# Kernel tuning notes

Measured on AMD Instinct MI355X. Metric: run time of the kernel, lower is better.

## Reference

```python
import jax, jax.numpy as jnp
import numpy as np

EPS = 1e-5
KP_EXTENT = 0.05


def _lrelu(x):
    return jnp.where(x >= 0, x, 0.1 * x)


def _bn(x, g, b, m, v):
    return g * (x - m) * jax.lax.rsqrt(v + EPS) + b


def setup_inputs() -> dict:
    key = jax.random.key(0)
    ks = jax.random.split(key, 20)
    N, K, P = 40000, 32, 15
    C_in, mid, C_out = 128, 64, 256
    inp = {}
    inp["features"] = jax.random.normal(ks[0], (N, C_in), dtype=jnp.float32)
    # points in a small cube so neighbor distances ~ KP_radius (0.06)
    inp["points"] = jax.random.uniform(ks[1], (N, 3), dtype=jnp.float32) * 0.1
    inp["neighbor_idx"] = jax.random.randint(ks[2], (N, K), 0, N, dtype=jnp.int32)
    # main path: Conv1D(in->mid) + BN
    inp["W1"] = jax.random.normal(ks[3], (C_in, mid), dtype=jnp.float32) * (1.0 / np.sqrt(C_in))
    inp["bn1_g"] = 1.0 + 0.1 * jax.random.normal(ks[4], (mid,), dtype=jnp.float32)
    inp["bn1_b"] = 0.1 * jax.random.normal(ks[5], (mid,), dtype=jnp.float32)
    inp["bn1_m"] = 0.1 * jax.random.normal(ks[6], (mid,), dtype=jnp.float32)
    inp["bn1_v"] = 0.5 + 0.5 * jax.random.uniform(ks[7], (mid,), dtype=jnp.float32)
    # KPConv: fixed kernel point positions in ball of radius 0.06, weights [P, mid, mid]
    inp["kernel_points"] = jax.random.normal(ks[8], (P, 3), dtype=jnp.float32) * 0.03
    inp["Wkp"] = jax.random.normal(ks[9], (P, mid, mid), dtype=jnp.float32) * (1.0 / np.sqrt(P * mid))
    # Conv1D(mid->out) + BN
    inp["W2"] = jax.random.normal(ks[10], (mid, C_out), dtype=jnp.float32) * (1.0 / np.sqrt(mid))
    inp["bn2_g"] = 1.0 + 0.1 * jax.random.normal(ks[11], (C_out,), dtype=jnp.float32)
    inp["bn2_b"] = 0.1 * jax.random.normal(ks[12], (C_out,), dtype=jnp.float32)
    inp["bn2_m"] = 0.1 * jax.random.normal(ks[13], (C_out,), dtype=jnp.float32)
    inp["bn2_v"] = 0.5 + 0.5 * jax.random.uniform(ks[14], (C_out,), dtype=jnp.float32)
    # shortcut Conv1D(in->out) + BN
    inp["Ws"] = jax.random.normal(ks[15], (C_in, C_out), dtype=jnp.float32) * (1.0 / np.sqrt(C_in))
    inp["bns_g"] = 1.0 + 0.1 * jax.random.normal(ks[16], (C_out,), dtype=jnp.float32)
    inp["bns_b"] = 0.1 * jax.random.normal(ks[17], (C_out,), dtype=jnp.float32)
    inp["bns_m"] = 0.1 * jax.random.normal(ks[18], (C_out,), dtype=jnp.float32)
    inp["bns_v"] = 0.5 + 0.5 * jax.random.uniform(ks[19], (C_out,), dtype=jnp.float32)
    return inp


def reference(features, points, neighbor_idx,
              W1, bn1_g, bn1_b, bn1_m, bn1_v,
              kernel_points, Wkp,
              W2, bn2_g, bn2_b, bn2_m, bn2_v,
              Ws, bns_g, bns_b, bns_m, bns_v):
    # --- main path ---
    # Conv1D: pointwise linear + BN(eval) + LeakyReLU
    x = _lrelu(_bn(features @ W1, bn1_g, bn1_b, bn1_m, bn1_v))  # [N, mid]
    # KPConvNeighbors (rigid KPConv, linear influence)
    f_n = x[neighbor_idx]                                # [N, K, mid] gather
    d = points[neighbor_idx] - points[:, None, :]        # [N, K, 3]
    diff = d[:, :, None, :] - kernel_points[None, None]  # [N, K, P, 3]
    dist = jnp.sqrt(jnp.sum(diff * diff, axis=-1))       # [N, K, P]
    h = jnp.maximum(0.0, 1.0 - dist / KP_EXTENT)         # influence [N, K, P]
    wf = jnp.einsum('nkp,nkc->npc', h, f_n)              # [N, P, mid]
    y = jnp.einsum('npc,pcd->nd', wf, Wkp)               # [N, mid]
    y = _lrelu(y)
    y = _lrelu(_bn(y @ W2, bn2_g, bn2_b, bn2_m, bn2_v))  # [N, C_out]
    # --- shortcut ---
    sc = _lrelu(_bn(features @ Ws, bns_g, bns_b, bns_m, bns_v))
    # residual add + final leaky relu
    return _lrelu(y + sc)
```

## Files before the change

### kernel.cpp

```cpp
#include <hip/hip_runtime.h>
#include <math.h>

#define EPSBN 1e-5f

constexpr int CIN  = 128;
constexpr int MID  = 64;
constexpr int COUT = 256;
constexpr int KNB  = 32;
constexpr int PKP  = 15;

constexpr int PSTR = 72;
constexpr int WROW = PKP * PSTR;
constexpr int YROW = 72;

typedef __bf16 v8bf  __attribute__((ext_vector_type(8)));
typedef float  f32x4 __attribute__((ext_vector_type(4)));

__device__ __forceinline__ float lrelu(float x) { return x >= 0.0f ? x : 0.1f * x; }

__device__ __forceinline__ void split1(float v, unsigned short& h, unsigned short& l) {
    __bf16 hb = (__bf16)v;
    float r = v - (float)hb;
    __bf16 lb = (__bf16)r;
    h = __builtin_bit_cast(unsigned short, hb);
    l = __builtin_bit_cast(unsigned short, lb);
}

__device__ __forceinline__ void split_frag8(const float* s, v8bf& hi, v8bf& lo) {
    #pragma unroll
    for (int j = 0; j < 8; ++j) {
        __bf16 hb = (__bf16)s[j];
        float r = s[j] - (float)hb;
        hi[j] = hb;
        lo[j] = (__bf16)r;
    }
}

__device__ __forceinline__ v8bf as_v8bf(uint4 u) {
    union { uint4 u; v8bf v; } X;
    X.u = u;
    return X.v;
}

__device__ __forceinline__ unsigned bf16_rne(float f) {
    unsigned u = __float_as_uint(f);
    return (u + 0x7fffu + ((u >> 16) & 1u)) >> 16;
}
__device__ __forceinline__ void split_pack8(const float* s, v8bf& hi, v8bf& lo) {
    unsigned h[8], l[8];
    #pragma unroll
    for (int j = 0; j < 8; ++j) {
        float a = s[j];
        unsigned hu = bf16_rne(a);
        float r = a - __uint_as_float(hu << 16);
        h[j] = hu;
        l[j] = bf16_rne(r);
    }
    union { uint4 u; v8bf v; } H, L;
    H.u = make_uint4(h[0] | (h[1] << 16), h[2] | (h[3] << 16),
                     h[4] | (h[5] << 16), h[6] | (h[7] << 16));
    L.u = make_uint4(l[0] | (l[1] << 16), l[2] | (l[3] << 16),
                     l[4] | (l[5] << 16), l[6] | (l[7] << 16));
    hi = H.v;
    lo = L.v;
}

__global__ __launch_bounds__(256) void prep(
    const float* __restrict__ Wkp, const float* __restrict__ W1,
    const float* __restrict__ Ws,  const float* __restrict__ W2,
    const float* __restrict__ g1, const float* __restrict__ b1,
    const float* __restrict__ m1, const float* __restrict__ v1,
    const float* __restrict__ gs, const float* __restrict__ bs,
    const float* __restrict__ ms, const float* __restrict__ vs,
    const float* __restrict__ g2, const float* __restrict__ b2,
    const float* __restrict__ m2, const float* __restrict__ v2,
    uint4* __restrict__ WkpPh, uint4* __restrict__ WkpPl,
    uint4* __restrict__ WcPh,  uint4* __restrict__ WcPl,
    uint4* __restrict__ W2Ph,  uint4* __restrict__ W2Pl,
    float* __restrict__ bnscale, float* __restrict__ bnshift)
{
    const int b = blockIdx.x, t = threadIdx.x;
    if (b < 30) {
        int gt = b * 256 + t;
        int lane = gt & 63, rest = gt >> 6;
        int nt = rest & 3, kt = rest >> 2;
        int col = nt * 16 + (lane & 15);
        int kbase = kt * 32 + ((lane >> 4) << 3);
        float tmp[8];
        #pragma unroll
        for (int j = 0; j < 8; ++j)
            tmp[j] = Wkp[(size_t)(kbase + j) * MID + col];
        v8bf hi, lo;
        split_pack8(tmp, hi, lo);
        union { v8bf v; uint4 u; } H, L; H.v = hi; L.v = lo;
        WkpPh[gt] = H.u; WkpPl[gt] = L.u;
    } else if (b < 50) {
        int gt = (b - 30) * 256 + t;
        int lane = gt & 63, rest = gt >> 6;
        int kt = rest / 20, nt = rest % 20;
        int c = nt * 16 + (lane & 15);
        int kbase = kt * 32 + ((lane >> 4) << 3);
        float tmp[8];
        #pragma unroll
        for (int j = 0; j < 8; ++j) {
            int k = kbase + j;
            tmp[j] = (c < 64) ? W1[(size_t)k * MID + c]
                              : Ws[(size_t)k * COUT + (c - 64)];
        }
        v8bf hi, lo;
        split_pack8(tmp, hi, lo);
        union { v8bf v; uint4 u; } H, L; H.v = hi; L.v = lo;
        WcPh[gt] = H.u; WcPl[gt] = L.u;
    } else if (b < 58) {
        int gt = (b - 50) * 256 + t;
        int lane = gt & 63, rest = gt >> 6;
        int kt = rest >> 4, nt = rest & 15;
        int col = nt * 16 + (lane & 15);
        int kbase = kt * 32 + ((lane >> 4) << 3);
        float tmp[8];
        #pragma unroll
        for (int j = 0; j < 8; ++j)
            tmp[j] = W2[(size_t)(kbase + j) * COUT + col];
        v8bf hi, lo;
        split_pack8(tmp, hi, lo);
        union { v8bf v; uint4 u; } H, L; H.v = hi; L.v = lo;
        W2Ph[gt] = H.u; W2Pl[gt] = L.u;
    } else {
        int v = (b - 58) * 256 + t;
        if (v < 576) {
            float g, bb, mm, vv;
            if (v < 64)       { g = g1[v]; bb = b1[v]; mm = m1[v]; vv = v1[v]; }
            else if (v < 320) { int c = v - 64;  g = gs[c]; bb = bs[c]; mm = ms[c]; vv = vs[c]; }
            else              { int c = v - 320; g = g2[c]; bb = b2[c]; mm = m2[c]; vv = v2[c]; }
            float s = g / sqrtf(vv + EPSBN);
            bnscale[v] = s;
            bnshift[v] = bb - mm * s;
        }
    }
}

__global__ __launch_bounds__(256) void k1_mfma(
    const float* __restrict__ F,
    const uint4* __restrict__ WcPh, const uint4* __restrict__ WcPl,
    const float* __restrict__ bnscale, const float* __restrict__ bnshift,
    unsigned* __restrict__ xp, float* __restrict__ scbuf)
{
    __shared__ float As[64][132];
    const int t = threadIdx.x;
    const int n0 = blockIdx.x * 64;

    const float4* src = (const float4*)(F + (size_t)n0 * CIN);
    #pragma unroll
    for (int i = 0; i < 8; ++i) {
        int idx = t + 256 * i;
        int row = idx >> 5, c4 = idx & 31;
        float4 v = src[idx];
        *(float4*)&As[row][c4 * 4] = v;
    }
    __syncthreads();

    const int l = t & 63, w = t >> 6;
    const int arow = w * 16 + (l & 15);
    const int k8 = (l >> 4) * 8;

    f32x4 acc[20];
    #pragma unroll
    for (int nt = 0; nt < 20; ++nt) acc[nt] = (f32x4){0.f, 0.f, 0.f, 0.f};

    #pragma unroll
    for (int kt = 0; kt < 4; ++kt) {
        float tmp[8];
        const float* ap = &As[arow][kt * 32 + k8];
        #pragma unroll
        for (int j = 0; j < 8; ++j) tmp[j] = ap[j];
        v8bf ah, al;
        split_frag8(tmp, ah, al);
        #pragma unroll
        for (int nt = 0; nt < 20; ++nt) {
            int bidx = ((kt * 20 + nt) << 6) + l;
            v8bf bh = as_v8bf(WcPh[bidx]);
            v8bf bl = as_v8bf(WcPl[bidx]);
            acc[nt] = __builtin_amdgcn_mfma_f32_16x16x32_bf16(ah, bh, acc[nt], 0, 0, 0);
            acc[nt] = __builtin_amdgcn_mfma_f32_16x16x32_bf16(al, bh, acc[nt], 0, 0, 0);
            acc[nt] = __builtin_amdgcn_mfma_f32_16x16x32_bf16(ah, bl, acc[nt], 0, 0, 0);
        }
    }

    const int colr = l & 15;
    const int rq = (l >> 4) * 4;
    #pragma unroll
    for (int nt = 0; nt < 20; ++nt) {
        int col = nt * 16 + colr;
        float sc = bnscale[col], sh = bnshift[col];
        #pragma unroll
        for (int r = 0; r < 4; ++r) {
            int row = n0 + w * 16 + rq + r;
            float val = lrelu(acc[nt][r] * sc + sh);
            if (col < 64) {
                unsigned short hu, lu;
                split1(val, hu, lu);
                xp[(size_t)row * MID + col] = ((unsigned)hu << 16) | lu;
            } else {
                scbuf[(size_t)row * COUT + (col - 64)] = val;
            }
        }
    }
}

__global__ __launch_bounds__(256) void k234_fused(
    const unsigned* __restrict__ xp,
    const float* __restrict__ pts,
    const int* __restrict__ nidx,
    const float* __restrict__ kpp,
    const uint4* __restrict__ WkpPh, const uint4* __restrict__ WkpPl,
    const uint4* __restrict__ W2Ph,  const uint4* __restrict__ W2Pl,
    const float* __restrict__ bnscale, const float* __restrict__ bnshift,
    const float* __restrict__ scbuf,
    float* __restrict__ out)
{
    __shared__ unsigned short wfsH[16 * WROW];
    __shared__ unsigned short wfsL[16 * WROW];
    __shared__ unsigned short yH[16 * YROW];
    __shared__ unsigned short yL[16 * YROW];

    const int t = threadIdx.x;
    const int l = t & 63, w = t >> 6;
    const int col = l & 15, kg = l >> 4;
    const int k8 = kg * 8;
    const int n0 = blockIdx.x * 16;

    float kx = 0.f, ky = 0.f, kz = 0.f;
    if (col < PKP) { kx = kpp[col * 3]; ky = kpp[col * 3 + 1]; kz = kpp[col * 3 + 2]; }

    for (int pt = 0; pt < 4; ++pt) {
        const int pl = w * 4 + pt;
        const int n  = n0 + pl;
        const float cx = pts[(size_t)n * 3];
        const float cy = pts[(size_t)n * 3 + 1];
        const float cz = pts[(size_t)n * 3 + 2];
        const int4 nba = ((const int4*)nidx)[(size_t)n * 8 + kg * 2];
        const int4 nbb = ((const int4*)nidx)[(size_t)n * 8 + kg * 2 + 1];
        int nb[8] = {nba.x, nba.y, nba.z, nba.w, nbb.x, nbb.y, nbb.z, nbb.w};

        unsigned u[8][4];
        #pragma unroll
        for (int j = 0; j < 8; ++j) {
            const unsigned* xr = xp + (size_t)nb[j] * MID + col;
            u[j][0] = xr[0];
            u[j][1] = xr[16];
            u[j][2] = xr[32];
            u[j][3] = xr[48];
        }

        float hv[8];
        #pragma unroll
        for (int j = 0; j < 8; ++j) {
            float ex = (pts[(size_t)nb[j] * 3]     - cx) - kx;
            float ey = (pts[(size_t)nb[j] * 3 + 1] - cy) - ky;
            float ez = (pts[(size_t)nb[j] * 3 + 2] - cz) - kz;
            float dist = sqrtf(ex * ex + ey * ey + ez * ez);
            float h = fmaxf(0.0f, 1.0f - dist * 20.0f);
            hv[j] = (col < PKP) ? h : 0.0f;
        }
        v8bf ah, al;
        split_frag8(hv, ah, al);

        #pragma unroll
        for (int nt = 0; nt < 4; ++nt) {
            unsigned bhW[4], blW[4];
            #pragma unroll
            for (int i = 0; i < 4; ++i) {
                unsigned u0 = u[2 * i][nt], u1 = u[2 * i + 1][nt];
                bhW[i] = (u1 & 0xFFFF0000u) | (u0 >> 16);
                blW[i] = (u1 << 16) | (u0 & 0xFFFFu);
            }
            v8bf bh = as_v8bf(make_uint4(bhW[0], bhW[1], bhW[2], bhW[3]));
            v8bf bl = as_v8bf(make_uint4(blW[0], blW[1], blW[2], blW[3]));
            f32x4 acc = {0.f, 0.f, 0.f, 0.f};
            acc = __builtin_amdgcn_mfma_f32_16x16x32_bf16(ah, bh, acc, 0, 0, 0);
            acc = __builtin_amdgcn_mfma_f32_16x16x32_bf16(al, bh, acc, 0, 0, 0);
            acc = __builtin_amdgcn_mfma_f32_16x16x32_bf16(ah, bl, acc, 0, 0, 0);
            #pragma unroll
            for (int r = 0; r < 4; ++r) {
                int p = kg * 4 + r;
                if (p < PKP) {
                    unsigned short hu, lu;
                    split1(acc[r], hu, lu);
                    int off = pl * WROW + p * PSTR + nt * 16 + col;
                    wfsH[off] = hu;
                    wfsL[off] = lu;
                }
            }
        }
    }
    __syncthreads();

    f32x4 a0 = {0.f, 0.f, 0.f, 0.f};
    f32x4 a1 = {0.f, 0.f, 0.f, 0.f};
    f32x4 a2 = {0.f, 0.f, 0.f, 0.f};
    #pragma unroll
    for (int kt = 0; kt < 30; ++kt) {
        int koff = col * WROW + (kt >> 1) * PSTR + (kt & 1) * 32 + k8;
        v8bf ah = as_v8bf(*(const uint4*)&wfsH[koff]);
        v8bf al = as_v8bf(*(const uint4*)&wfsL[koff]);
        int bidx = ((kt << 2) + w) * 64 + l;
        v8bf bh = as_v8bf(WkpPh[bidx]);
        v8bf bl = as_v8bf(WkpPl[bidx]);
        a0 = __builtin_amdgcn_mfma_f32_16x16x32_bf16(ah, bh, a0, 0, 0, 0);
        a1 = __builtin_amdgcn_mfma_f32_16x16x32_bf16(al, bh, a1, 0, 0, 0);
        a2 = __builtin_amdgcn_mfma_f32_16x16x32_bf16(ah, bl, a2, 0, 0, 0);
    }
    #pragma unroll
    for (int r = 0; r < 4; ++r) {
        float yv = lrelu(a0[r] + a1[r] + a2[r]);
        unsigned short hu, lu;
        split1(yv, hu, lu);
        int off = (kg * 4 + r) * YROW + w * 16 + col;
        yH[off] = hu;
        yL[off] = lu;
    }
    __syncthreads();

    f32x4 acc2[4];
    #pragma unroll
    for (int i = 0; i < 4; ++i) acc2[i] = (f32x4){0.f, 0.f, 0.f, 0.f};
    #pragma unroll
    for (int kt = 0; kt < 2; ++kt) {
        int yoff = col * YROW + kt * 32 + k8;
        v8bf ah = as_v8bf(*(const uint4*)&yH[yoff]);
        v8bf al = as_v8bf(*(const uint4*)&yL[yoff]);
        #pragma unroll
        for (int ntl = 0; ntl < 4; ++ntl) {
            int nt2 = w * 4 + ntl;
            int bidx = (((kt << 4) + nt2) << 6) + l;
            v8bf bh = as_v8bf(W2Ph[bidx]);
            v8bf bl = as_v8bf(W2Pl[bidx]);
            acc2[ntl] = __builtin_amdgcn_mfma_f32_16x16x32_bf16(ah, bh, acc2[ntl], 0, 0, 0);
            acc2[ntl] = __builtin_amdgcn_mfma_f32_16x16x32_bf16(al, bh, acc2[ntl], 0, 0, 0);
            acc2[ntl] = __builtin_amdgcn_mfma_f32_16x16x32_bf16(ah, bl, acc2[ntl], 0, 0, 0);
        }
    }
    #pragma unroll
    for (int ntl = 0; ntl < 4; ++ntl) {
        int cold = (w * 4 + ntl) * 16 + col;
        float sc = bnscale[320 + cold], sh = bnshift[320 + cold];
        #pragma unroll
        for (int r = 0; r < 4; ++r) {
            int n = n0 + kg * 4 + r;
            float val = lrelu(acc2[ntl][r] * sc + sh);
            float scv = scbuf[(size_t)n * COUT + cold];
            out[(size_t)n * COUT + cold] = lrelu(val + scv);
        }
    }
}

extern "C" void kernel_launch(void* const* d_in, const int* in_sizes, int n_in,
                              void* d_out, int out_size, void* d_ws, size_t ws_size,
                              hipStream_t stream)
{
    const float* F   = (const float*)d_in[0];
    const float* pts = (const float*)d_in[1];
    const int*   nid = (const int*)d_in[2];
    const float* W1  = (const float*)d_in[3];
    const float* g1  = (const float*)d_in[4];
    const float* b1  = (const float*)d_in[5];
    const float* m1  = (const float*)d_in[6];
    const float* v1  = (const float*)d_in[7];
    const float* kpp = (const float*)d_in[8];
    const float* Wkp = (const float*)d_in[9];
    const float* W2  = (const float*)d_in[10];
    const float* g2  = (const float*)d_in[11];
    const float* b2  = (const float*)d_in[12];
    const float* m2  = (const float*)d_in[13];
    const float* v2  = (const float*)d_in[14];
    const float* Ws  = (const float*)d_in[15];
    const float* gs  = (const float*)d_in[16];
    const float* bs  = (const float*)d_in[17];
    const float* ms  = (const float*)d_in[18];
    const float* vs  = (const float*)d_in[19];

    const int N = in_sizes[0] / CIN;

    unsigned* xp   = (unsigned*)d_ws;
    float* scbuf   = (float*)(xp + (size_t)N * MID);
    uint4* WkpPh   = (uint4*)(scbuf + (size_t)N * COUT);
    uint4* WkpPl   = WkpPh + 7680;
    uint4* WcPh    = WkpPl + 7680;
    uint4* WcPl    = WcPh + 5120;
    uint4* W2Ph    = WcPl + 5120;
    uint4* W2Pl    = W2Ph + 2048;
    float* bnscale = (float*)(W2Pl + 2048);
    float* bnshift = bnscale + 576;
    float* out     = (float*)d_out;

    prep<<<61, 256, 0, stream>>>(Wkp, W1, Ws, W2,
                                 g1, b1, m1, v1, gs, bs, ms, vs, g2, b2, m2, v2,
                                 WkpPh, WkpPl, WcPh, WcPl, W2Ph, W2Pl,
                                 bnscale, bnshift);
    k1_mfma<<<N / 64, 256, 0, stream>>>(F, WcPh, WcPl, bnscale, bnshift, xp, scbuf);
    k234_fused<<<N / 16, 256, 0, stream>>>(xp, pts, nid, kpp,
                                           WkpPh, WkpPl, W2Ph, W2Pl,
                                           bnscale, bnshift, scbuf, out);
}
```

Measured before the change: 237.0 us.

## Split k1 output columns across grid and double k234 threads with split-K

Result: faster. 220.9 us (-6.8%).

```diff
diff --git a/kernel.cpp b/kernel.cpp
--- a/kernel.cpp
+++ b/kernel.cpp
@@ -145,39 +145,35 @@
     const float* __restrict__ bnscale, const float* __restrict__ bnshift,
     unsigned* __restrict__ xp, float* __restrict__ scbuf)
 {
-    __shared__ float As[64][132];
     const int t = threadIdx.x;
+    const int l = t & 63, w = t >> 6;
     const int n0 = blockIdx.x * 64;
-
-    const float4* src = (const float4*)(F + (size_t)n0 * CIN);
-    #pragma unroll
-    for (int i = 0; i < 8; ++i) {
-        int idx = t + 256 * i;
-        int row = idx >> 5, c4 = idx & 31;
-        float4 v = src[idx];
-        *(float4*)&As[row][c4 * 4] = v;
-    }
-    __syncthreads();
-
-    const int l = t & 63, w = t >> 6;
-    const int arow = w * 16 + (l & 15);
-    const int k8 = (l >> 4) * 8;
-
-    f32x4 acc[20];
-    #pragma unroll
-    for (int nt = 0; nt < 20; ++nt) acc[nt] = (f32x4){0.f, 0.f, 0.f, 0.f};
-
+    const int ntbase = blockIdx.y * 10;
+    const int colr = l & 15, kg = l >> 4;
+    const int arow = n0 + w * 16 + colr;
+    const int k8 = kg * 8;
+
+    const float* fr = F + (size_t)arow * CIN + k8;
+    float4 av[4][2];
     #pragma unroll
     for (int kt = 0; kt < 4; ++kt) {
-        float tmp[8];
-        const float* ap = &As[arow][kt * 32 + k8];
-        #pragma unroll
-        for (int j = 0; j < 8; ++j) tmp[j] = ap[j];
+        av[kt][0] = *(const float4*)(fr + kt * 32);
+        av[kt][1] = *(const float4*)(fr + kt * 32 + 4);
+    }
+
+    f32x4 acc[10];
+    #pragma unroll
+    for (int nt = 0; nt < 10; ++nt) acc[nt] = (f32x4){0.f, 0.f, 0.f, 0.f};
+
+    #pragma unroll
+    for (int kt = 0; kt < 4; ++kt) {
+        float tmp[8] = {av[kt][0].x, av[kt][0].y, av[kt][0].z, av[kt][0].w,
+                        av[kt][1].x, av[kt][1].y, av[kt][1].z, av[kt][1].w};
         v8bf ah, al;
         split_frag8(tmp, ah, al);
         #pragma unroll
-        for (int nt = 0; nt < 20; ++nt) {
-            int bidx = ((kt * 20 + nt) << 6) + l;
+        for (int nt = 0; nt < 10; ++nt) {
+            int bidx = ((kt * 20 + ntbase + nt) << 6) + l;
             v8bf bh = as_v8bf(WcPh[bidx]);
             v8bf bl = as_v8bf(WcPl[bidx]);
             acc[nt] = __builtin_amdgcn_mfma_f32_16x16x32_bf16(ah, bh, acc[nt], 0, 0, 0);
@@ -186,11 +182,10 @@
         }
     }
 
-    const int colr = l & 15;
-    const int rq = (l >> 4) * 4;
-    #pragma unroll
-    for (int nt = 0; nt < 20; ++nt) {
-        int col = nt * 16 + colr;
+    const int rq = kg * 4;
+    #pragma unroll
+    for (int nt = 0; nt < 10; ++nt) {
+        int col = (ntbase + nt) * 16 + colr;
         float sc = bnscale[col], sh = bnshift[col];
         #pragma unroll
         for (int r = 0; r < 4; ++r) {
@@ -207,7 +202,7 @@
     }
 }
 
-__global__ __launch_bounds__(256) void k234_fused(
+__global__ __launch_bounds__(512) void k234_fused(
     const unsigned* __restrict__ xp,
     const float* __restrict__ pts,
     const int* __restrict__ nidx,
@@ -220,6 +215,7 @@
 {
     __shared__ unsigned short wfsH[16 * WROW];
     __shared__ unsigned short wfsL[16 * WROW];
+    __shared__ float         yP[4][16][17];
     __shared__ unsigned short yH[16 * YROW];
     __shared__ unsigned short yL[16 * YROW];
 
@@ -232,8 +228,8 @@
     float kx = 0.f, ky = 0.f, kz = 0.f;
     if (col < PKP) { kx = kpp[col * 3]; ky = kpp[col * 3 + 1]; kz = kpp[col * 3 + 2]; }
 
-    for (int pt = 0; pt < 4; ++pt) {
-        const int pl = w * 4 + pt;
+    for (int pt = 0; pt < 2; ++pt) {
+        const int pl = w * 2 + pt;
         const int n  = n0 + pl;
         const float cx = pts[(size_t)n * 3];
         const float cy = pts[(size_t)n * 3 + 1];
@@ -295,59 +291,70 @@
     }
     __syncthreads();
 
+    const int nt = w & 3;
+    const int khalf = w >> 2;
     f32x4 a0 = {0.f, 0.f, 0.f, 0.f};
     f32x4 a1 = {0.f, 0.f, 0.f, 0.f};
     f32x4 a2 = {0.f, 0.f, 0.f, 0.f};
     #pragma unroll
-    for (int kt = 0; kt < 30; ++kt) {
+    for (int i = 0; i < 15; ++i) {
+        int kt = khalf * 15 + i;
         int koff = col * WROW + (kt >> 1) * PSTR + (kt & 1) * 32 + k8;
         v8bf ah = as_v8bf(*(const uint4*)&wfsH[koff]);
         v8bf al = as_v8bf(*(const uint4*)&wfsL[koff]);
-        int bidx = ((kt << 2) + w) * 64 + l;
+        int bidx = ((kt << 2) + nt) * 64 + l;
         v8bf bh = as_v8bf(WkpPh[bidx]);
         v8bf bl = as_v8bf(WkpPl[bidx]);
         a0 = __builtin_amdgcn_mfma_f32_16x16x32_bf16(ah, bh, a0, 0, 0, 0);
         a1 = __builtin_amdgcn_mfma_f32_16x16x32_bf16(al, bh, a1, 0, 0, 0);
         a2 = __builtin_amdgcn_mfma_f32_16x16x32_bf16(ah, bl, a2, 0, 0, 0);
     }
-    #pragma unroll
-    for (int r = 0; r < 4; ++r) {
-        float yv = lrelu(a0[r] + a1[r] + a2[r]);
-        unsigned short hu, lu;
-        split1(yv, hu, lu);
-        int off = (kg * 4 + r) * YROW + w * 16 + col;
-        yH[off] = hu;
-        yL[off] = lu;
+    if (khalf == 1) {
+        #pragma unroll
+        for (int r = 0; r < 4; ++r)
+            yP[nt][kg * 4 + r][col] = a0[r] + a1[r] + a2[r];
     }
     __syncthreads();
-
-    f32x4 acc2[4];
-    #pragma unroll
-    for (int i = 0; i < 4; ++i) acc2[i] = (f32x4){0.f, 0.f, 0.f, 0.f};
+    if (khalf == 0) {
+        #pragma unroll
+        for (int r = 0; r < 4; ++r) {
+            float yv = lrelu(a0[r] + a1[r] + a2[r] + yP[nt][kg * 4 + r][col]);
+            unsigned short hu, lu;
+            split1(yv, hu, lu);
+            int off = (kg * 4 + r) * YROW + nt * 16 + col;
+            yH[off] = hu;
+            yL[off] = lu;
+        }
+    }
+    __syncthreads();
+
+    f32x4 acc2[2];
+    #pragma unroll
+    for (int i = 0; i < 2; ++i) acc2[i] = (f32x4){0.f, 0.f, 0.f, 0.f};
     #pragma unroll
     for (int kt = 0; kt < 2; ++kt) {
         int yoff = col * YROW + kt * 32 + k8;
         v8bf ah = as_v8bf(*(const uint4*)&yH[yoff]);
         v8bf al = as_v8bf(*(const uint4*)&yL[yoff]);
         #pragma unroll
-        for (int ntl = 0; ntl < 4; ++ntl) {
-            int nt2 = w * 4 + ntl;
+        for (int ii = 0; ii < 2; ++ii) {
+            int nt2 = w * 2 + ii;
             int bidx = (((kt << 4) + nt2) << 6) + l;
             v8bf bh = as_v8bf(W2Ph[bidx]);
             v8bf bl = as_v8bf(W2Pl[bidx]);
-            acc2[ntl] = __builtin_amdgcn_mfma_f32_16x16x32_bf16(ah, bh, acc2[ntl], 0, 0, 0);
-            acc2[ntl] = __builtin_amdgcn_mfma_f32_16x16x32_bf16(al, bh, acc2[ntl], 0, 0, 0);
-            acc2[ntl] = __builtin_amdgcn_mfma_f32_16x16x32_bf16(ah, bl, acc2[ntl], 0, 0, 0);
-        }
-    }
-    #pragma unroll
-    for (int ntl = 0; ntl < 4; ++ntl) {
-        int cold = (w * 4 + ntl) * 16 + col;
+            acc2[ii] = __builtin_amdgcn_mfma_f32_16x16x32_bf16(ah, bh, acc2[ii], 0, 0, 0);
+            acc2[ii] = __builtin_amdgcn_mfma_f32_16x16x32_bf16(al, bh, acc2[ii], 0, 0, 0);
+            acc2[ii] = __builtin_amdgcn_mfma_f32_16x16x32_bf16(ah, bl, acc2[ii], 0, 0, 0);
+        }
+    }
+    #pragma unroll
+    for (int ii = 0; ii < 2; ++ii) {
+        int cold = (w * 2 + ii) * 16 + col;
         float sc = bnscale[320 + cold], sh = bnshift[320 + cold];
         #pragma unroll
         for (int r = 0; r < 4; ++r) {
             int n = n0 + kg * 4 + r;
-            float val = lrelu(acc2[ntl][r] * sc + sh);
+            float val = lrelu(acc2[ii][r] * sc + sh);
             float scv = scbuf[(size_t)n * COUT + cold];
             out[(size_t)n * COUT + cold] = lrelu(val + scv);
         }
@@ -397,8 +404,8 @@
                                  g1, b1, m1, v1, gs, bs, ms, vs, g2, b2, m2, v2,
                                  WkpPh, WkpPl, WcPh, WcPl, W2Ph, W2Pl,
                                  bnscale, bnshift);
-    k1_mfma<<<N / 64, 256, 0, stream>>>(F, WcPh, WcPl, bnscale, bnshift, xp, scbuf);
-    k234_fused<<<N / 16, 256, 0, stream>>>(xp, pts, nid, kpp,
+    k1_mfma<<<dim3(N / 64, 2), 256, 0, stream>>>(F, WcPh, WcPl, bnscale, bnshift, xp, scbuf);
+    k234_fused<<<N / 16, 512, 0, stream>>>(xp, pts, nid, kpp,
                                            WkpPh, WkpPl, W2Ph, W2Pl,
                                            bnscale, bnshift, scbuf, out);
 }
```
